# Optimization experiments

Measured on AMD Instinct MI355X. Metric: run time of the kernel, lower is better.

Reference implementation:

```python
import jax, jax.numpy as jnp
import numpy as np

H, N, BSZ, L = 512, 64, 8, 2048
DT_MIN, DT_MAX = 1e-3, 1e-1


def _hippo_dplr(n_state):
    """HiPPO-LegS -> DPLR (Lambda, P, B) init, as in the Annotated S4."""
    n = np.arange(n_state, dtype=np.float64)
    p = np.sqrt(n + 0.5)                      # low-rank factor P
    pm = np.sqrt(1.0 + 2.0 * n)
    A = np.tril(pm[:, None] * pm[None, :]) - np.diag(n)
    A = -A                                    # HiPPO-LegS A
    S = A + p[:, None] * p[None, :]           # normal part (skew-symmetric + cI)
    lam_real = np.mean(np.diagonal(S)) * np.ones(n_state)
    lam_imag, V = np.linalg.eigh(S * -1j)
    Lam = lam_real + 1j * lam_imag
    B = np.sqrt(2.0 * n + 1.0)
    return Lam, V.conj().T @ p, V.conj().T @ B


def setup_inputs() -> dict:
    key = jax.random.key(0)
    k1, k2, k3, k4, k5 = jax.random.split(key, 5)
    Lam, P, B = _hippo_dplr(N)
    return {
        "u": jax.random.normal(k1, (BSZ, L, H), dtype=jnp.float32),
        "Lambda_real": jnp.asarray(Lam.real, jnp.float32),
        "Lambda_imag": jnp.asarray(Lam.imag, jnp.float32),
        "P_real": jnp.asarray(P.real, jnp.float32),
        "P_imag": jnp.asarray(P.imag, jnp.float32),
        "B_real": jnp.asarray(B.real, jnp.float32),
        "B_imag": jnp.asarray(B.imag, jnp.float32),
        "C_real": jax.random.normal(k2, (H, N), jnp.float32) * 0.5,
        "C_imag": jax.random.normal(k3, (H, N), jnp.float32) * 0.5,
        "log_dt": jax.random.uniform(k4, (H,), jnp.float32,
                                     float(np.log(DT_MIN)), float(np.log(DT_MAX))),
        "D": jax.random.normal(k5, (H,), jnp.float32) * 0.01,
    }


def _s4_forward(u, Lr, Li, Pr, Pi, Br, Bi, Cr, Ci, log_dt, D):
    Lam = (Lr + 1j * Li).astype(jnp.complex64)   # (N,)
    P = (Pr + 1j * Pi).astype(jnp.complex64)     # (N,)
    B = (Br + 1j * Bi).astype(jnp.complex64)     # (N,)
    C = (Cr + 1j * Ci).astype(jnp.complex64)     # (H, N)
    l_len = u.shape[1]
    dt = jnp.exp(log_dt)                         # (H,)

    # --- DPLR kernel via Cauchy-kernel generating function (bilinear disc),
    # batched over all H channels instead of the per-channel Python loop. ---
    omega = jnp.exp(-2j * jnp.pi * jnp.arange(l_len, dtype=jnp.float32) / l_len)
    omega = omega.astype(jnp.complex64)          # roots of unity, (L,)
    g = (2.0 / dt)[:, None].astype(jnp.complex64) * ((1.0 - omega) / (1.0 + omega))[None, :]  # (H, L)
    c2 = 2.0 / (1.0 + omega)                     # (L,)
    r = 1.0 / (g[:, :, None] - Lam[None, None, :])  # Cauchy resolvent (H, L, N)
    Cc = jnp.conj(C)                             # (H, N)
    Qc = jnp.conj(P)                             # (N,)
    k00 = jnp.einsum('hn,hln->hl', Cc * B[None, :], r)
    k01 = jnp.einsum('hn,hln->hl', Cc * P[None, :], r)
    k10 = jnp.einsum('n,hln->hl', Qc * B, r)
    k11 = jnp.einsum('n,hln->hl', Qc * P, r)
    at_roots = c2[None, :] * (k00 - k01 * k10 / (1.0 + k11))  # (H, L)
    K = jnp.fft.ifft(at_roots, axis=-1).real.astype(u.dtype)  # (H, L) conv kernel

    # --- causal FFT convolution per channel ---
    x = jnp.swapaxes(u, -1, -2)                  # (B, H, L)
    n_fft = 2 * l_len
    Xf = jnp.fft.rfft(x, n=n_fft)
    Kf = jnp.fft.rfft(K, n=n_fft)
    y = jnp.fft.irfft(Xf * Kf[None], n=n_fft)[..., :l_len]
    y = y + x * D[None, :, None]                 # skip connection
    return jnp.swapaxes(y, -1, -2)               # (B, L, H)


def reference(u, Lambda_real, Lambda_imag, P_real, P_imag, B_real, B_imag,
              C_real, C_imag, log_dt, D):
    return _s4_forward(u, Lambda_real, Lambda_imag, P_real, P_imag,
                       B_real, B_imag, C_real, C_imag, log_dt, D)
```

## Files before the change

### kernel.cpp

```cpp
#include <hip/hip_runtime.h>
#include <math.h>

#define LSEQ 2048
#define HCH  512
#define NST  64
#define NBATCH 8
#define PIf 3.14159265358979f

#define PHYS(i) ((i) + ((i) >> 3))
#define LDSN 2304

__device__ __forceinline__ float2 cmul(float2 a, float2 b) {
    return make_float2(a.x * b.x - a.y * b.y, a.x * b.y + a.y * b.x);
}
__device__ __forceinline__ float2 cadd(float2 a, float2 b) { return make_float2(a.x + b.x, a.y + b.y); }
__device__ __forceinline__ float2 csub(float2 a, float2 b) { return make_float2(a.x - b.x, a.y - b.y); }
__device__ __forceinline__ float2 csq(float2 a) { return make_float2(a.x * a.x - a.y * a.y, 2.f * a.x * a.y); }
template<int INV>
__device__ __forceinline__ float2 rot90(float2 a) {
    return INV ? make_float2(-a.y, a.x) : make_float2(a.y, -a.x);
}

template<int INV, int STAGE>
__device__ __forceinline__ void radix8_pass(const float2* __restrict__ src,
                                            float2* __restrict__ dst, int tid)
{
    const int Ns  = 1 << STAGE;
    const int lam = tid & (Ns - 1);
    const int G   = ((tid >> STAGE) << (STAGE + 3)) + lam;

    float2 x0 = src[PHYS(tid)];
    float2 x1 = src[PHYS(tid + 256)];
    float2 x2 = src[PHYS(tid + 512)];
    float2 x3 = src[PHYS(tid + 768)];
    float2 x4 = src[PHYS(tid + 1024)];
    float2 x5 = src[PHYS(tid + 1280)];
    float2 x6 = src[PHYS(tid + 1536)];
    float2 x7 = src[PHYS(tid + 1792)];

    const float SGN = INV ? 1.f : -1.f;
    float sn, cs;
    __sincosf(SGN * (PIf / (float)(4 * Ns)) * (float)lam, &sn, &cs);
    const float2 T3 = make_float2(cs, sn);
    const float2 T2 = csq(T3);
    const float2 T1 = csq(T2);
    const float r2 = 0.70710678118f;
    const float2 U = cmul(T3, make_float2(r2, SGN * r2));

    float2 t;
    t = cmul(T1, x4); float2 a0 = cadd(x0, t), a4 = csub(x0, t);
    t = cmul(T1, x5); float2 a1 = cadd(x1, t), a5 = csub(x1, t);
    t = cmul(T1, x6); float2 a2 = cadd(x2, t), a6 = csub(x2, t);
    t = cmul(T1, x7); float2 a3 = cadd(x3, t), a7 = csub(x3, t);
    t = cmul(T2, a2);             float2 b0 = cadd(a0, t), b2 = csub(a0, t);
    t = cmul(T2, a3);             float2 b1 = cadd(a1, t), b3 = csub(a1, t);
    t = rot90<INV>(cmul(T2, a6)); float2 b4 = cadd(a4, t), b6 = csub(a4, t);
    t = rot90<INV>(cmul(T2, a7)); float2 b5 = cadd(a5, t), b7 = csub(a5, t);
    t = cmul(T3, b1);             dst[PHYS(G)]          = cadd(b0, t); dst[PHYS(G + 4 * Ns)] = csub(b0, t);
    t = rot90<INV>(cmul(T3, b3)); dst[PHYS(G + 2 * Ns)] = cadd(b2, t); dst[PHYS(G + 6 * Ns)] = csub(b2, t);
    t = cmul(U, b5);              dst[PHYS(G + Ns)]     = cadd(b4, t); dst[PHYS(G + 5 * Ns)] = csub(b4, t);
    t = rot90<INV>(cmul(U, b7));  dst[PHYS(G + 3 * Ns)] = cadd(b6, t); dst[PHYS(G + 7 * Ns)] = csub(b6, t);
}

template<int INV>
__device__ float2* fft2048(float2* bufA, float2* bufB)
{
    const int tid = threadIdx.x;
    __syncthreads();
    radix8_pass<INV, 0>(bufA, bufB, tid);
    __syncthreads();
    radix8_pass<INV, 3>(bufB, bufA, tid);
    __syncthreads();
    radix8_pass<INV, 6>(bufA, bufB, tid);
    __syncthreads();
    const float SGN = INV ? 1.f : -1.f;
#pragma unroll
    for (int q = 0; q < 2; ++q) {
        const int j = tid + (q << 8);
        float2 A  = bufB[PHYS(j)];
        float2 C  = bufB[PHYS(j + 512)];
        float2 B  = bufB[PHYS(j + 1024)];
        float2 Dd = bufB[PHYS(j + 1536)];
        float sn, cs;
        __sincosf(SGN * (PIf / 1024.f) * (float)j, &sn, &cs);
        const float2 v = make_float2(cs, sn);
        const float2 w = csq(v);
        float2 t = cmul(w, B);  float2 m1 = cadd(A, t), m2 = csub(A, t);
        t = cmul(w, Dd);        float2 m3 = cadd(C, t), m4 = csub(C, t);
        const float2 t3 = cmul(v, m3);
        const float2 t4 = rot90<INV>(cmul(v, m4));
        bufA[PHYS(j)]        = cadd(m1, t3);
        bufA[PHYS(j + 1024)] = csub(m1, t3);
        bufA[PHYS(j + 512)]  = cadd(m2, t4);
        bufA[PHYS(j + 1536)] = csub(m2, t4);
    }
    __syncthreads();
    return bufA;
}

__global__ __launch_bounds__(256, 4)
void s4_cauchy_kernel(const float* __restrict__ Lr, const float* __restrict__ Li,
                      const float* __restrict__ Pr, const float* __restrict__ Pi,
                      const float* __restrict__ Br, const float* __restrict__ Bi,
                      const float* __restrict__ Cr, const float* __restrict__ Ci,
                      const float* __restrict__ log_dt, float2* __restrict__ at_out)
{
    __shared__ float4 F0[NST];
    __shared__ float4 F1[NST];
    __shared__ float  q1s[NST];

    const int h    = blockIdx.x >> 1;
    const int half = blockIdx.x & 1;
    const int tid  = threadIdx.x;

    if (tid < NST) {
        const float pr = Pr[tid], pi = Pi[tid], br = Br[tid], bi = Bi[tid];
        const float cr = Cr[h * NST + tid], ci = Ci[h * NST + tid];
        F0[tid]  = make_float4(Lr[tid], Li[tid], cr * br + ci * bi, cr * bi - ci * br);
        F1[tid]  = make_float4(cr * pr + ci * pi, cr * pi - ci * pr,
                               pr * br + pi * bi, pr * bi - pi * br);
        q1s[tid] = pr * pr + pi * pi;
    }
    __syncthreads();

    const float dt = expf(log_dt[h]);
    const float a  = 2.0f / dt;

    float tt[4], g[4];
#pragma unroll
    for (int p = 0; p < 4; ++p) {
        const int l = (half << 10) + (p << 8) + tid;
        tt[p] = tanf(PIf * (float)l * (1.0f / 2048.0f));
        g[p]  = a * tt[p];
    }

    float k00r[4], k00i[4], k01r[4], k01i[4];
    float k10r[4], k10i[4], k11r[4], k11i[4];
#pragma unroll
    for (int p = 0; p < 4; ++p) {
        k00r[p] = 0.f; k00i[p] = 0.f; k01r[p] = 0.f; k01i[p] = 0.f;
        k10r[p] = 0.f; k10i[p] = 0.f; k11r[p] = 0.f; k11i[p] = 0.f;
    }

#pragma unroll 2
    for (int n = 0; n < NST; ++n) {
        const float4 f0 = F0[n];
        const float4 f1 = F1[n];
        const float q1 = q1s[n];
        const float x  = -f0.x;
        const float x2 = x * x;
#pragma unroll
        for (int p = 0; p < 4; ++p) {
            const float y   = g[p] - f0.y;
            const float inv = __builtin_amdgcn_rcpf(fmaf(y, y, x2));
            const float rr  = x * inv;
            const float ri  = -y * inv;
            k00r[p] = fmaf(f0.z, rr, fmaf(-f0.w, ri, k00r[p]));
            k00i[p] = fmaf(f0.z, ri, fmaf( f0.w, rr, k00i[p]));
            k01r[p] = fmaf(f1.x, rr, fmaf(-f1.y, ri, k01r[p]));
            k01i[p] = fmaf(f1.x, ri, fmaf( f1.y, rr, k01i[p]));
            k10r[p] = fmaf(f1.z, rr, fmaf(-f1.w, ri, k10r[p]));
            k10i[p] = fmaf(f1.z, ri, fmaf( f1.w, rr, k10i[p]));
            k11r[p] = fmaf(q1, rr, k11r[p]);
            k11i[p] = fmaf(q1, ri, k11i[p]);
        }
    }

    float2* __restrict__ row = at_out + (size_t)h * 2048;
#pragma unroll
    for (int p = 0; p < 4; ++p) {
        const int l = (half << 10) + (p << 8) + tid;
        const float dr = 1.0f + k11r[p], di = k11i[p];
        const float dinv = __builtin_amdgcn_rcpf(fmaf(dr, dr, di * di));
        const float pr_ = k01r[p] * k10r[p] - k01i[p] * k10i[p];
        const float pi_ = k01r[p] * k10i[p] + k01i[p] * k10r[p];
        const float qr = (pr_ * dr + pi_ * di) * dinv;
        const float qi = (pi_ * dr - pr_ * di) * dinv;
        const float sr = k00r[p] - qr, si = k00i[p] - qi;
        row[l] = make_float2(fmaf(-tt[p], si, sr), fmaf(tt[p], sr, si));
    }
}

__global__ __launch_bounds__(256, 4)
void s4_kf_kernel(const float2* __restrict__ at_in, float2* __restrict__ Kf)
{
    __shared__ float2 bufA[LDSN];
    __shared__ float2 bufB[LDSN];

    const int h   = blockIdx.x;
    const int tid = threadIdx.x;
    const float2* __restrict__ at = at_in + (size_t)h * 2048;

    for (int q = 0; q < 8; ++q) {
        const int l = tid + (q << 8);
        bufA[PHYS(l)] = at[l];
    }

    float2* Kt = fft2048<1>(bufA, bufB);

    const float sc = 1.0f / 2048.0f;
    for (int n = tid; n < 1024; n += 256)
        bufB[PHYS(n)] = make_float2(Kt[PHYS(2 * n)].x * sc, Kt[PHYS(2 * n + 1)].x * sc);
    for (int n = 1024 + tid; n < 2048; n += 256)
        bufB[PHYS(n)] = make_float2(0.f, 0.f);

    float2* Z = fft2048<0>(bufB, bufA);

    float2* __restrict__ out = Kf + (size_t)h * 2049;
    for (int k = tid; k < 1024; k += 256) {
        const float2 Zk = Z[PHYS(k)];
        const float2 Zm = Z[PHYS((2048 - k) & 2047)];
        const float zer = 0.5f * (Zk.x + Zm.x), zei = 0.5f * (Zk.y - Zm.y);
        const float zdr = Zk.x - Zm.x,         zdi = Zk.y + Zm.y;
        const float zor = 0.5f * zdi,          zoi = -0.5f * zdr;
        float s, c;
        __sincosf(-PIf * (float)k * (1.0f / 2048.0f), &s, &c);
        const float txr = c * zor - s * zoi;
        const float txi = c * zoi + s * zor;
        out[k] = make_float2(zer + txr, zei + txi);
        if (k > 0) {
            out[2048 - k] = make_float2(zer - txr, txi - zei);
        } else {
            out[2048] = make_float2(Zk.x - Zk.y, 0.f);
        }
    }
    if (tid == 0) {
        const float2 z = Z[PHYS(1024)];
        out[1024] = make_float2(z.x, -z.y);
    }
}

__global__ __launch_bounds__(256, 4)
void s4_conv_kernel(const float* __restrict__ u, float* ws_rows,
                    const float2* __restrict__ Kf, const float* __restrict__ Dv,
                    float* __restrict__ out, int fastpath)
{
    __shared__ float2 bufA[LDSN];
    __shared__ float2 bufB[LDSN];
    __shared__ float2 yfN;

    const int bh  = blockIdx.x;
    const int b   = bh >> 9;
    const int h   = bh & 511;
    const int tid = threadIdx.x;

    if (fastpath) {
        const float2* rowv = (const float2*)(ws_rows + (size_t)bh * LSEQ);
        for (int n = tid; n < 1024; n += 256) bufA[PHYS(n)] = rowv[n];
    } else {
        const float* ub = u + (size_t)b * LSEQ * HCH + h;
        for (int n = tid; n < 1024; n += 256)
            bufA[PHYS(n)] = make_float2(ub[(size_t)(2 * n) * HCH],
                                        ub[(size_t)(2 * n + 1) * HCH]);
    }
    for (int n = 1024 + tid; n < 2048; n += 256) bufA[PHYS(n)] = make_float2(0.f, 0.f);

    float2* Z  = fft2048<0>(bufA, bufB);
    float2* NB = bufB;
    const float2* __restrict__ kf = Kf + (size_t)h * 2049;

    for (int k = tid; k < 1024; k += 256) {
        const float2 Zk = Z[PHYS(k)];
        const float2 Zm = Z[PHYS((2048 - k) & 2047)];
        const float zer = 0.5f * (Zk.x + Zm.x), zei = 0.5f * (Zk.y - Zm.y);
        const float zdr = Zk.x - Zm.x,          zdi = Zk.y + Zm.y;
        const float zor = 0.5f * zdi,           zoi = -0.5f * zdr;
        float s, c;
        __sincosf(-PIf * (float)k * (1.0f / 2048.0f), &s, &c);
        const float txr = c * zor - s * zoi;
        const float txi = c * zoi + s * zor;
        const float xr = zer + txr, xi = zei + txi;
        const float2 kk = kf[k];
        NB[PHYS(k)] = make_float2(xr * kk.x - xi * kk.y, xr * kk.y + xi * kk.x);
        if (k > 0) {
            const float mr = zer - txr, mi = txi - zei;
            const float2 km = kf[2048 - k];
            NB[PHYS(2048 - k)] = make_float2(mr * km.x - mi * km.y,
                                             mr * km.y + mi * km.x);
        } else {
            const float x2048 = Zk.x - Zk.y;
            const float2 k2 = kf[2048];
            yfN = make_float2(x2048 * k2.x, x2048 * k2.y);
        }
    }
    if (tid == 0) {
        const float2 z  = Z[PHYS(1024)];
        const float2 kk = kf[1024];
        NB[PHYS(1024)] = make_float2(z.x * kk.x + z.y * kk.y,
                                     z.x * kk.y - z.y * kk.x);
    }
    __syncthreads();

    for (int k = tid; k < 1024; k += 256) {
        const float2 Yk = NB[PHYS(k)];
        const float2 Ym = (k == 0) ? yfN : NB[PHYS(2048 - k)];
        const float yer = 0.5f * (Yk.x + Ym.x), yei = 0.5f * (Yk.y - Ym.y);
        const float ydr = Yk.x - Ym.x,          ydi = Yk.y + Ym.y;
        float s, c;
        __sincosf(PIf * (float)k * (1.0f / 2048.0f), &s, &c);
        const float yor = 0.5f * (c * ydr - s * ydi);
        const float yoi = 0.5f * (c * ydi + s * ydr);
        bufA[PHYS(k)] = make_float2(yer - yoi, yei + yor);
        if (k > 0) {
            const float yer2 = 0.5f * (Ym.x + Yk.x), yei2 = 0.5f * (Ym.y - Yk.y);
            const float ydr2 = Ym.x - Yk.x,          ydi2 = Ym.y + Yk.y;
            const float yor2 = 0.5f * (-c * ydr2 - s * ydi2);
            const float yoi2 = 0.5f * (-c * ydi2 + s * ydr2);
            bufA[PHYS(2048 - k)] = make_float2(yer2 - yoi2, yei2 + yor2);
        }
    }
    if (tid == 0) {
        const float2 Y = NB[PHYS(1024)];
        bufA[PHYS(1024)] = make_float2(Y.x, -Y.y);
    }

    float2* w = fft2048<1>(bufA, bufB);
    const float Dh = Dv[h];
    const float sc = 1.0f / 2048.0f;
    if (fastpath) {
        float2* rowv = (float2*)(ws_rows + (size_t)bh * LSEQ);
        for (int n = tid; n < 1024; n += 256) {
            const float2 wv = w[PHYS(n)];
            const float2 xv = rowv[n];
            rowv[n] = make_float2(wv.x * sc + Dh * xv.x,
                                  wv.y * sc + Dh * xv.y);
        }
    } else {
        const float* ub = u + (size_t)b * LSEQ * HCH + h;
        float* ob = out + (size_t)b * LSEQ * HCH + h;
        for (int n = tid; n < 1024; n += 256) {
            const float2 wv = w[PHYS(n)];
            ob[(size_t)(2 * n) * HCH]     = wv.x * sc + Dh * ub[(size_t)(2 * n) * HCH];
            ob[(size_t)(2 * n + 1) * HCH] = wv.y * sc + Dh * ub[(size_t)(2 * n + 1) * HCH];
        }
    }
}

__global__ __launch_bounds__(256)
void transpose_kernel(const float* __restrict__ in, float* __restrict__ out,
                      int rows, int cols)
{
    __shared__ float tile[32][33];
    const int b  = blockIdx.z;
    const int r0 = blockIdx.y << 5;
    const int c0 = blockIdx.x << 5;
    const size_t base = (size_t)b * rows * cols;
    const int tx = threadIdx.x & 31;
    const int ty = threadIdx.x >> 5;
#pragma unroll
    for (int i = 0; i < 32; i += 8)
        tile[ty + i][tx] = in[base + (size_t)(r0 + ty + i) * cols + (c0 + tx)];
    __syncthreads();
#pragma unroll
    for (int i = 0; i < 32; i += 8)
        out[base + (size_t)(c0 + ty + i) * rows + (r0 + tx)] = tile[tx][ty + i];
}

extern "C" void kernel_launch(void* const* d_in, const int* in_sizes, int n_in,
                              void* d_out, int out_size, void* d_ws, size_t ws_size,
                              hipStream_t stream)
{
    (void)in_sizes; (void)n_in; (void)out_size;
    const float* u  = (const float*)d_in[0];
    const float* Lr = (const float*)d_in[1];
    const float* Li = (const float*)d_in[2];
    const float* Pr = (const float*)d_in[3];
    const float* Pi = (const float*)d_in[4];
    const float* Br = (const float*)d_in[5];
    const float* Bi = (const float*)d_in[6];
    const float* Cr = (const float*)d_in[7];
    const float* Ci = (const float*)d_in[8];
    const float* ld = (const float*)d_in[9];
    const float* Dv = (const float*)d_in[10];
    float* out = (float*)d_out;

    const size_t UT_BYTES = (size_t)NBATCH * HCH * LSEQ * sizeof(float);
    const size_t KF_BYTES = (size_t)HCH * 2049 * sizeof(float2);
    const int fast = (ws_size >= UT_BYTES + KF_BYTES) ? 1 : 0;

    float*  ut;
    float2* Kf;
    if (fast) { ut = (float*)d_ws; Kf = (float2*)((char*)d_ws + UT_BYTES); }
    else      { ut = (float*)d_ws; Kf = (float2*)d_ws; }

    float2* at = (float2*)d_out;

    hipLaunchKernelGGL(s4_cauchy_kernel, dim3(HCH * 2), dim3(256), 0, stream,
                       Lr, Li, Pr, Pi, Br, Bi, Cr, Ci, ld, at);
    hipLaunchKernelGGL(s4_kf_kernel, dim3(HCH), dim3(256), 0, stream, at, Kf);
    if (fast) {
        hipLaunchKernelGGL(transpose_kernel, dim3(HCH / 32, LSEQ / 32, NBATCH),
                           dim3(256), 0, stream, u, ut, LSEQ, HCH);
    }
    hipLaunchKernelGGL(s4_conv_kernel, dim3(NBATCH * HCH), dim3(256), 0, stream,
                       u, fast ? ut : nullptr, Kf, Dv, out, fast);
    if (fast) {
        hipLaunchKernelGGL(transpose_kernel, dim3(LSEQ / 32, HCH / 32, NBATCH),
                           dim3(256), 0, stream, ut, out, HCH, LSEQ);
    }
}
```

Measured before the change: 115.9 us.

## Make conv-kernel FFTs in-place with a single LDS buffer for higher occupancy

```diff
diff --git a/kernel.cpp b/kernel.cpp
--- a/kernel.cpp
+++ b/kernel.cpp
@@ -98,6 +98,82 @@
     return bufA;
 }
 
+template<int INV, int STAGE>
+__device__ __forceinline__ void radix8_inplace(float2* __restrict__ buf, int tid)
+{
+    __syncthreads();
+    float2 x0 = buf[PHYS(tid)];
+    float2 x1 = buf[PHYS(tid + 256)];
+    float2 x2 = buf[PHYS(tid + 512)];
+    float2 x3 = buf[PHYS(tid + 768)];
+    float2 x4 = buf[PHYS(tid + 1024)];
+    float2 x5 = buf[PHYS(tid + 1280)];
+    float2 x6 = buf[PHYS(tid + 1536)];
+    float2 x7 = buf[PHYS(tid + 1792)];
+    __syncthreads();
+
+    const int Ns  = 1 << STAGE;
+    const int lam = tid & (Ns - 1);
+    const int G   = ((tid >> STAGE) << (STAGE + 3)) + lam;
+    const float SGN = INV ? 1.f : -1.f;
+    float sn, cs;
+    __sincosf(SGN * (PIf / (float)(4 * Ns)) * (float)lam, &sn, &cs);
+    const float2 T3 = make_float2(cs, sn);
+    const float2 T2 = csq(T3);
+    const float2 T1 = csq(T2);
+    const float r2 = 0.70710678118f;
+    const float2 U = cmul(T3, make_float2(r2, SGN * r2));
+    float2 t;
+    t = cmul(T1, x4); float2 a0 = cadd(x0, t), a4 = csub(x0, t);
+    t = cmul(T1, x5); float2 a1 = cadd(x1, t), a5 = csub(x1, t);
+    t = cmul(T1, x6); float2 a2 = cadd(x2, t), a6 = csub(x2, t);
+    t = cmul(T1, x7); float2 a3 = cadd(x3, t), a7 = csub(x3, t);
+    t = cmul(T2, a2);             float2 b0 = cadd(a0, t), b2 = csub(a0, t);
+    t = cmul(T2, a3);             float2 b1 = cadd(a1, t), b3 = csub(a1, t);
+    t = rot90<INV>(cmul(T2, a6)); float2 b4 = cadd(a4, t), b6 = csub(a4, t);
+    t = rot90<INV>(cmul(T2, a7)); float2 b5 = cadd(a5, t), b7 = csub(a5, t);
+    t = cmul(T3, b1);             buf[PHYS(G)]          = cadd(b0, t); buf[PHYS(G + 4 * Ns)] = csub(b0, t);
+    t = rot90<INV>(cmul(T3, b3)); buf[PHYS(G + 2 * Ns)] = cadd(b2, t); buf[PHYS(G + 6 * Ns)] = csub(b2, t);
+    t = cmul(U, b5);              buf[PHYS(G + Ns)]     = cadd(b4, t); buf[PHYS(G + 5 * Ns)] = csub(b4, t);
+    t = rot90<INV>(cmul(U, b7));  buf[PHYS(G + 3 * Ns)] = cadd(b6, t); buf[PHYS(G + 7 * Ns)] = csub(b6, t);
+}
+
+template<int INV>
+__device__ __forceinline__ void radix4_inplace(float2* __restrict__ buf, int tid)
+{
+    __syncthreads();
+    const float SGN = INV ? 1.f : -1.f;
+#pragma unroll
+    for (int q = 0; q < 2; ++q) {
+        const int j = tid + (q << 8);
+        float2 A  = buf[PHYS(j)];
+        float2 C  = buf[PHYS(j + 512)];
+        float2 B  = buf[PHYS(j + 1024)];
+        float2 Dd = buf[PHYS(j + 1536)];
+        float sn, cs;
+        __sincosf(SGN * (PIf / 1024.f) * (float)j, &sn, &cs);
+        const float2 v = make_float2(cs, sn);
+        const float2 w = csq(v);
+        float2 t = cmul(w, B);  float2 m1 = cadd(A, t), m2 = csub(A, t);
+        t = cmul(w, Dd);        float2 m3 = cadd(C, t), m4 = csub(C, t);
+        const float2 t3 = cmul(v, m3);
+        const float2 t4 = rot90<INV>(cmul(v, m4));
+        buf[PHYS(j)]        = cadd(m1, t3);
+        buf[PHYS(j + 1024)] = csub(m1, t3);
+        buf[PHYS(j + 512)]  = cadd(m2, t4);
+        buf[PHYS(j + 1536)] = csub(m2, t4);
+    }
+}
+
+template<int INV>
+__device__ __forceinline__ void fft2048_ip(float2* buf, int tid)
+{
+    radix8_inplace<INV, 0>(buf, tid);
+    radix8_inplace<INV, 3>(buf, tid);
+    radix8_inplace<INV, 6>(buf, tid);
+    radix4_inplace<INV>(buf, tid);
+}
+
 __global__ __launch_bounds__(256, 4)
 void s4_cauchy_kernel(const float* __restrict__ Lr, const float* __restrict__ Li,
                       const float* __restrict__ Pr, const float* __restrict__ Pi,
@@ -230,13 +306,12 @@
     }
 }
 
-__global__ __launch_bounds__(256, 4)
+__global__ __launch_bounds__(256, 6)
 void s4_conv_kernel(const float* __restrict__ u, float* ws_rows,
                     const float2* __restrict__ Kf, const float* __restrict__ Dv,
                     float* __restrict__ out, int fastpath)
 {
-    __shared__ float2 bufA[LDSN];
-    __shared__ float2 bufB[LDSN];
+    __shared__ float2 buf[LDSN];
     __shared__ float2 yfN;
 
     const int bh  = blockIdx.x;
@@ -246,24 +321,35 @@
 
     if (fastpath) {
         const float2* rowv = (const float2*)(ws_rows + (size_t)bh * LSEQ);
-        for (int n = tid; n < 1024; n += 256) bufA[PHYS(n)] = rowv[n];
+        for (int n = tid; n < 1024; n += 256) buf[PHYS(n)] = rowv[n];
     } else {
         const float* ub = u + (size_t)b * LSEQ * HCH + h;
         for (int n = tid; n < 1024; n += 256)
-            bufA[PHYS(n)] = make_float2(ub[(size_t)(2 * n) * HCH],
-                                        ub[(size_t)(2 * n + 1) * HCH]);
-    }
-    for (int n = 1024 + tid; n < 2048; n += 256) bufA[PHYS(n)] = make_float2(0.f, 0.f);
-
-    float2* Z  = fft2048<0>(bufA, bufB);
-    float2* NB = bufB;
+            buf[PHYS(n)] = make_float2(ub[(size_t)(2 * n) * HCH],
+                                       ub[(size_t)(2 * n + 1) * HCH]);
+    }
+    for (int n = 1024 + tid; n < 2048; n += 256) buf[PHYS(n)] = make_float2(0.f, 0.f);
+
+    fft2048_ip<0>(buf, tid);
+
     const float2* __restrict__ kf = Kf + (size_t)h * 2049;
 
-    for (int k = tid; k < 1024; k += 256) {
-        const float2 Zk = Z[PHYS(k)];
-        const float2 Zm = Z[PHYS((2048 - k) & 2047)];
-        const float zer = 0.5f * (Zk.x + Zm.x), zei = 0.5f * (Zk.y - Zm.y);
-        const float zdr = Zk.x - Zm.x,          zdi = Zk.y + Zm.y;
+    __syncthreads();
+    float2 Zk[4], Zm[4], Z1024v;
+#pragma unroll
+    for (int q = 0; q < 4; ++q) {
+        const int k = tid + (q << 8);
+        Zk[q] = buf[PHYS(k)];
+        Zm[q] = buf[PHYS((2048 - k) & 2047)];
+    }
+    if (tid == 0) Z1024v = buf[PHYS(1024)];
+    __syncthreads();
+#pragma unroll
+    for (int q = 0; q < 4; ++q) {
+        const int k = tid + (q << 8);
+        const float2 zk = Zk[q], zm = Zm[q];
+        const float zer = 0.5f * (zk.x + zm.x), zei = 0.5f * (zk.y - zm.y);
+        const float zdr = zk.x - zm.x,          zdi = zk.y + zm.y;
         const float zor = 0.5f * zdi,           zoi = -0.5f * zdr;
         float s, c;
         __sincosf(-PIf * (float)k * (1.0f / 2048.0f), &s, &c);
@@ -271,56 +357,66 @@
         const float txi = c * zoi + s * zor;
         const float xr = zer + txr, xi = zei + txi;
         const float2 kk = kf[k];
-        NB[PHYS(k)] = make_float2(xr * kk.x - xi * kk.y, xr * kk.y + xi * kk.x);
+        buf[PHYS(k)] = make_float2(xr * kk.x - xi * kk.y, xr * kk.y + xi * kk.x);
         if (k > 0) {
             const float mr = zer - txr, mi = txi - zei;
             const float2 km = kf[2048 - k];
-            NB[PHYS(2048 - k)] = make_float2(mr * km.x - mi * km.y,
-                                             mr * km.y + mi * km.x);
+            buf[PHYS(2048 - k)] = make_float2(mr * km.x - mi * km.y,
+                                              mr * km.y + mi * km.x);
         } else {
-            const float x2048 = Zk.x - Zk.y;
+            const float x2048 = zk.x - zk.y;
             const float2 k2 = kf[2048];
             yfN = make_float2(x2048 * k2.x, x2048 * k2.y);
         }
     }
     if (tid == 0) {
-        const float2 z  = Z[PHYS(1024)];
         const float2 kk = kf[1024];
-        NB[PHYS(1024)] = make_float2(z.x * kk.x + z.y * kk.y,
-                                     z.x * kk.y - z.y * kk.x);
-    }
-    __syncthreads();
-
-    for (int k = tid; k < 1024; k += 256) {
-        const float2 Yk = NB[PHYS(k)];
-        const float2 Ym = (k == 0) ? yfN : NB[PHYS(2048 - k)];
-        const float yer = 0.5f * (Yk.x + Ym.x), yei = 0.5f * (Yk.y - Ym.y);
-        const float ydr = Yk.x - Ym.x,          ydi = Yk.y + Ym.y;
+        buf[PHYS(1024)] = make_float2(Z1024v.x * kk.x + Z1024v.y * kk.y,
+                                      Z1024v.x * kk.y - Z1024v.y * kk.x);
+    }
+
+    __syncthreads();
+    float2 Yk[4], Ym[4], Y1024v;
+#pragma unroll
+    for (int q = 0; q < 4; ++q) {
+        const int k = tid + (q << 8);
+        Yk[q] = buf[PHYS(k)];
+        Ym[q] = (k == 0) ? yfN : buf[PHYS(2048 - k)];
+    }
+    if (tid == 0) Y1024v = buf[PHYS(1024)];
+    __syncthreads();
+#pragma unroll
+    for (int q = 0; q < 4; ++q) {
+        const int k = tid + (q << 8);
+        const float2 yk = Yk[q], ym = Ym[q];
+        const float yer = 0.5f * (yk.x + ym.x), yei = 0.5f * (yk.y - ym.y);
+        const float ydr = yk.x - ym.x,          ydi = yk.y + ym.y;
         float s, c;
         __sincosf(PIf * (float)k * (1.0f / 2048.0f), &s, &c);
         const float yor = 0.5f * (c * ydr - s * ydi);
         const float yoi = 0.5f * (c * ydi + s * ydr);
-        bufA[PHYS(k)] = make_float2(yer - yoi, yei + yor);
+        buf[PHYS(k)] = make_float2(yer - yoi, yei + yor);
         if (k > 0) {
-            const float yer2 = 0.5f * (Ym.x + Yk.x), yei2 = 0.5f * (Ym.y - Yk.y);
-            const float ydr2 = Ym.x - Yk.x,          ydi2 = Ym.y + Yk.y;
+            const float yer2 = 0.5f * (ym.x + yk.x), yei2 = 0.5f * (ym.y - yk.y);
+            const float ydr2 = ym.x - yk.x,          ydi2 = ym.y + yk.y;
             const float yor2 = 0.5f * (-c * ydr2 - s * ydi2);
             const float yoi2 = 0.5f * (-c * ydi2 + s * ydr2);
-            bufA[PHYS(2048 - k)] = make_float2(yer2 - yoi2, yei2 + yor2);
+            buf[PHYS(2048 - k)] = make_float2(yer2 - yoi2, yei2 + yor2);
         }
     }
     if (tid == 0) {
-        const float2 Y = NB[PHYS(1024)];
-        bufA[PHYS(1024)] = make_float2(Y.x, -Y.y);
-    }
-
-    float2* w = fft2048<1>(bufA, bufB);
+        buf[PHYS(1024)] = make_float2(Y1024v.x, -Y1024v.y);
+    }
+
+    fft2048_ip<1>(buf, tid);
+
+    __syncthreads();
     const float Dh = Dv[h];
     const float sc = 1.0f / 2048.0f;
     if (fastpath) {
         float2* rowv = (float2*)(ws_rows + (size_t)bh * LSEQ);
         for (int n = tid; n < 1024; n += 256) {
-            const float2 wv = w[PHYS(n)];
+            const float2 wv = buf[PHYS(n)];
             const float2 xv = rowv[n];
             rowv[n] = make_float2(wv.x * sc + Dh * xv.x,
                                   wv.y * sc + Dh * xv.y);
@@ -329,7 +425,7 @@
         const float* ub = u + (size_t)b * LSEQ * HCH + h;
         float* ob = out + (size_t)b * LSEQ * HCH + h;
         for (int n = tid; n < 1024; n += 256) {
-            const float2 wv = w[PHYS(n)];
+            const float2 wv = buf[PHYS(n)];
             ob[(size_t)(2 * n) * HCH]     = wv.x * sc + Dh * ub[(size_t)(2 * n) * HCH];
             ob[(size_t)(2 * n + 1) * HCH] = wv.y * sc + Dh * ub[(size_t)(2 * n + 1) * HCH];
         }
```

Result: faster. 110.6 us (-4.5%).

## Pack two batches into one complex 4096-point FFT and drop transposes

Applied to the files above, without the earlier changes.

```diff
diff --git a/kernel.cpp b/kernel.cpp
--- a/kernel.cpp
+++ b/kernel.cpp
@@ -9,6 +9,7 @@
 
 #define PHYS(i) ((i) + ((i) >> 3))
 #define LDSN 2304
+#define LDSN4 4608
 
 __device__ __forceinline__ float2 cmul(float2 a, float2 b) {
     return make_float2(a.x * b.x - a.y * b.y, a.x * b.y + a.y * b.x);
@@ -98,6 +99,46 @@
     return bufA;
 }
 
+template<int INV, int STAGE>
+__device__ __forceinline__ void radix8_ip4096(float2* __restrict__ buf, int tid)
+{
+    __syncthreads();
+    float2 x0 = buf[PHYS(tid)];
+    float2 x1 = buf[PHYS(tid + 512)];
+    float2 x2 = buf[PHYS(tid + 1024)];
+    float2 x3 = buf[PHYS(tid + 1536)];
+    float2 x4 = buf[PHYS(tid + 2048)];
+    float2 x5 = buf[PHYS(tid + 2560)];
+    float2 x6 = buf[PHYS(tid + 3072)];
+    float2 x7 = buf[PHYS(tid + 3584)];
+    __syncthreads();
+
+    const int Ns  = 1 << STAGE;
+    const int lam = tid & (Ns - 1);
+    const int G   = ((tid >> STAGE) << (STAGE + 3)) + lam;
+    const float SGN = INV ? 1.f : -1.f;
+    float sn, cs;
+    __sincosf(SGN * (PIf / (float)(4 * Ns)) * (float)lam, &sn, &cs);
+    const float2 T3 = make_float2(cs, sn);
+    const float2 T2 = csq(T3);
+    const float2 T1 = csq(T2);
+    const float r2 = 0.70710678118f;
+    const float2 U = cmul(T3, make_float2(r2, SGN * r2));
+    float2 t;
+    t = cmul(T1, x4); float2 a0 = cadd(x0, t), a4 = csub(x0, t);
+    t = cmul(T1, x5); float2 a1 = cadd(x1, t), a5 = csub(x1, t);
+    t = cmul(T1, x6); float2 a2 = cadd(x2, t), a6 = csub(x2, t);
+    t = cmul(T1, x7); float2 a3 = cadd(x3, t), a7 = csub(x3, t);
+    t = cmul(T2, a2);             float2 b0 = cadd(a0, t), b2 = csub(a0, t);
+    t = cmul(T2, a3);             float2 b1 = cadd(a1, t), b3 = csub(a1, t);
+    t = rot90<INV>(cmul(T2, a6)); float2 b4 = cadd(a4, t), b6 = csub(a4, t);
+    t = rot90<INV>(cmul(T2, a7)); float2 b5 = cadd(a5, t), b7 = csub(a5, t);
+    t = cmul(T3, b1);             buf[PHYS(G)]          = cadd(b0, t); buf[PHYS(G + 4 * Ns)] = csub(b0, t);
+    t = rot90<INV>(cmul(T3, b3)); buf[PHYS(G + 2 * Ns)] = cadd(b2, t); buf[PHYS(G + 6 * Ns)] = csub(b2, t);
+    t = cmul(U, b5);              buf[PHYS(G + Ns)]     = cadd(b4, t); buf[PHYS(G + 5 * Ns)] = csub(b4, t);
+    t = rot90<INV>(cmul(U, b7));  buf[PHYS(G + 3 * Ns)] = cadd(b6, t); buf[PHYS(G + 7 * Ns)] = csub(b6, t);
+}
+
 __global__ __launch_bounds__(256, 4)
 void s4_cauchy_kernel(const float* __restrict__ Lr, const float* __restrict__ Li,
                       const float* __restrict__ Pr, const float* __restrict__ Pi,
@@ -230,137 +271,71 @@
     }
 }
 
-__global__ __launch_bounds__(256, 4)
-void s4_conv_kernel(const float* __restrict__ u, float* ws_rows,
-                    const float2* __restrict__ Kf, const float* __restrict__ Dv,
-                    float* __restrict__ out, int fastpath)
-{
-    __shared__ float2 bufA[LDSN];
-    __shared__ float2 bufB[LDSN];
-    __shared__ float2 yfN;
-
-    const int bh  = blockIdx.x;
-    const int b   = bh >> 9;
-    const int h   = bh & 511;
+__global__ __launch_bounds__(512, 8)
+void s4_conv_kernel(const float* __restrict__ u, const float2* __restrict__ Kf,
+                    const float* __restrict__ Dv, float* __restrict__ out)
+{
+    __shared__ float2 buf[LDSN4];
+
+    const int bp  = blockIdx.x;
+    const int h   = bp & (HCH - 1);
+    const int b0  = (bp >> 9) << 1;
     const int tid = threadIdx.x;
 
-    if (fastpath) {
-        const float2* rowv = (const float2*)(ws_rows + (size_t)bh * LSEQ);
-        for (int n = tid; n < 1024; n += 256) bufA[PHYS(n)] = rowv[n];
-    } else {
-        const float* ub = u + (size_t)b * LSEQ * HCH + h;
-        for (int n = tid; n < 1024; n += 256)
-            bufA[PHYS(n)] = make_float2(ub[(size_t)(2 * n) * HCH],
-                                        ub[(size_t)(2 * n + 1) * HCH]);
-    }
-    for (int n = 1024 + tid; n < 2048; n += 256) bufA[PHYS(n)] = make_float2(0.f, 0.f);
-
-    float2* Z  = fft2048<0>(bufA, bufB);
-    float2* NB = bufB;
+    const float* __restrict__ u0 = u + (size_t)b0 * LSEQ * HCH + h;
+    const float* __restrict__ u1 = u0 + (size_t)LSEQ * HCH;
+
+#pragma unroll
+    for (int m = 0; m < 4; ++m) {
+        const int n = tid + (m << 9);
+        buf[PHYS(n)]        = make_float2(u0[(size_t)n * HCH], u1[(size_t)n * HCH]);
+        buf[PHYS(n + 2048)] = make_float2(0.f, 0.f);
+    }
+
+    radix8_ip4096<0, 0>(buf, tid);
+    radix8_ip4096<0, 3>(buf, tid);
+    radix8_ip4096<0, 6>(buf, tid);
+    radix8_ip4096<0, 9>(buf, tid);
+
     const float2* __restrict__ kf = Kf + (size_t)h * 2049;
-
-    for (int k = tid; k < 1024; k += 256) {
-        const float2 Zk = Z[PHYS(k)];
-        const float2 Zm = Z[PHYS((2048 - k) & 2047)];
-        const float zer = 0.5f * (Zk.x + Zm.x), zei = 0.5f * (Zk.y - Zm.y);
-        const float zdr = Zk.x - Zm.x,          zdi = Zk.y + Zm.y;
-        const float zor = 0.5f * zdi,           zoi = -0.5f * zdr;
-        float s, c;
-        __sincosf(-PIf * (float)k * (1.0f / 2048.0f), &s, &c);
-        const float txr = c * zor - s * zoi;
-        const float txi = c * zoi + s * zor;
-        const float xr = zer + txr, xi = zei + txi;
-        const float2 kk = kf[k];
-        NB[PHYS(k)] = make_float2(xr * kk.x - xi * kk.y, xr * kk.y + xi * kk.x);
-        if (k > 0) {
-            const float mr = zer - txr, mi = txi - zei;
-            const float2 km = kf[2048 - k];
-            NB[PHYS(2048 - k)] = make_float2(mr * km.x - mi * km.y,
-                                             mr * km.y + mi * km.x);
+    __syncthreads();
+#pragma unroll
+    for (int m = 0; m < 8; ++m) {
+        const int k = tid + (m << 9);
+        float2 C;
+        if (k <= 2048) {
+            C = kf[k];
         } else {
-            const float x2048 = Zk.x - Zk.y;
-            const float2 k2 = kf[2048];
-            yfN = make_float2(x2048 * k2.x, x2048 * k2.y);
+            const float2 km = kf[4096 - k];
+            C = make_float2(km.x, -km.y);
         }
-    }
-    if (tid == 0) {
-        const float2 z  = Z[PHYS(1024)];
-        const float2 kk = kf[1024];
-        NB[PHYS(1024)] = make_float2(z.x * kk.x + z.y * kk.y,
-                                     z.x * kk.y - z.y * kk.x);
-    }
-    __syncthreads();
-
-    for (int k = tid; k < 1024; k += 256) {
-        const float2 Yk = NB[PHYS(k)];
-        const float2 Ym = (k == 0) ? yfN : NB[PHYS(2048 - k)];
-        const float yer = 0.5f * (Yk.x + Ym.x), yei = 0.5f * (Yk.y - Ym.y);
-        const float ydr = Yk.x - Ym.x,          ydi = Yk.y + Ym.y;
-        float s, c;
-        __sincosf(PIf * (float)k * (1.0f / 2048.0f), &s, &c);
-        const float yor = 0.5f * (c * ydr - s * ydi);
-        const float yoi = 0.5f * (c * ydi + s * ydr);
-        bufA[PHYS(k)] = make_float2(yer - yoi, yei + yor);
-        if (k > 0) {
-            const float yer2 = 0.5f * (Ym.x + Yk.x), yei2 = 0.5f * (Ym.y - Yk.y);
-            const float ydr2 = Ym.x - Yk.x,          ydi2 = Ym.y + Yk.y;
-            const float yor2 = 0.5f * (-c * ydr2 - s * ydi2);
-            const float yoi2 = 0.5f * (-c * ydi2 + s * ydr2);
-            bufA[PHYS(2048 - k)] = make_float2(yer2 - yoi2, yei2 + yor2);
-        }
-    }
-    if (tid == 0) {
-        const float2 Y = NB[PHYS(1024)];
-        bufA[PHYS(1024)] = make_float2(Y.x, -Y.y);
-    }
-
-    float2* w = fft2048<1>(bufA, bufB);
+        buf[PHYS(k)] = cmul(buf[PHYS(k)], C);
+    }
+
+    radix8_ip4096<1, 0>(buf, tid);
+    radix8_ip4096<1, 3>(buf, tid);
+    radix8_ip4096<1, 6>(buf, tid);
+    radix8_ip4096<1, 9>(buf, tid);
+
+    __syncthreads();
     const float Dh = Dv[h];
-    const float sc = 1.0f / 2048.0f;
-    if (fastpath) {
-        float2* rowv = (float2*)(ws_rows + (size_t)bh * LSEQ);
-        for (int n = tid; n < 1024; n += 256) {
-            const float2 wv = w[PHYS(n)];
-            const float2 xv = rowv[n];
-            rowv[n] = make_float2(wv.x * sc + Dh * xv.x,
-                                  wv.y * sc + Dh * xv.y);
-        }
-    } else {
-        const float* ub = u + (size_t)b * LSEQ * HCH + h;
-        float* ob = out + (size_t)b * LSEQ * HCH + h;
-        for (int n = tid; n < 1024; n += 256) {
-            const float2 wv = w[PHYS(n)];
-            ob[(size_t)(2 * n) * HCH]     = wv.x * sc + Dh * ub[(size_t)(2 * n) * HCH];
-            ob[(size_t)(2 * n + 1) * HCH] = wv.y * sc + Dh * ub[(size_t)(2 * n + 1) * HCH];
-        }
-    }
-}
-
-__global__ __launch_bounds__(256)
-void transpose_kernel(const float* __restrict__ in, float* __restrict__ out,
-                      int rows, int cols)
-{
-    __shared__ float tile[32][33];
-    const int b  = blockIdx.z;
-    const int r0 = blockIdx.y << 5;
-    const int c0 = blockIdx.x << 5;
-    const size_t base = (size_t)b * rows * cols;
-    const int tx = threadIdx.x & 31;
-    const int ty = threadIdx.x >> 5;
-#pragma unroll
-    for (int i = 0; i < 32; i += 8)
-        tile[ty + i][tx] = in[base + (size_t)(r0 + ty + i) * cols + (c0 + tx)];
-    __syncthreads();
-#pragma unroll
-    for (int i = 0; i < 32; i += 8)
-        out[base + (size_t)(c0 + ty + i) * rows + (r0 + tx)] = tile[tx][ty + i];
+    const float sc = 1.0f / 4096.0f;
+    float* __restrict__ o0 = out + (size_t)b0 * LSEQ * HCH + h;
+    float* __restrict__ o1 = o0 + (size_t)LSEQ * HCH;
+#pragma unroll
+    for (int m = 0; m < 4; ++m) {
+        const int n = tid + (m << 9);
+        const float2 w = buf[PHYS(n)];
+        o0[(size_t)n * HCH] = fmaf(Dh, u0[(size_t)n * HCH], w.x * sc);
+        o1[(size_t)n * HCH] = fmaf(Dh, u1[(size_t)n * HCH], w.y * sc);
+    }
 }
 
 extern "C" void kernel_launch(void* const* d_in, const int* in_sizes, int n_in,
                               void* d_out, int out_size, void* d_ws, size_t ws_size,
                               hipStream_t stream)
 {
-    (void)in_sizes; (void)n_in; (void)out_size;
+    (void)in_sizes; (void)n_in; (void)out_size; (void)ws_size;
     const float* u  = (const float*)d_in[0];
     const float* Lr = (const float*)d_in[1];
     const float* Li = (const float*)d_in[2];
@@ -374,28 +349,12 @@
     const float* Dv = (const float*)d_in[10];
     float* out = (float*)d_out;
 
-    const size_t UT_BYTES = (size_t)NBATCH * HCH * LSEQ * sizeof(float);
-    const size_t KF_BYTES = (size_t)HCH * 2049 * sizeof(float2);
-    const int fast = (ws_size >= UT_BYTES + KF_BYTES) ? 1 : 0;
-
-    float*  ut;
-    float2* Kf;
-    if (fast) { ut = (float*)d_ws; Kf = (float2*)((char*)d_ws + UT_BYTES); }
-    else      { ut = (float*)d_ws; Kf = (float2*)d_ws; }
-
+    float2* Kf = (float2*)d_ws;
     float2* at = (float2*)d_out;
 
     hipLaunchKernelGGL(s4_cauchy_kernel, dim3(HCH * 2), dim3(256), 0, stream,
                        Lr, Li, Pr, Pi, Br, Bi, Cr, Ci, ld, at);
     hipLaunchKernelGGL(s4_kf_kernel, dim3(HCH), dim3(256), 0, stream, at, Kf);
-    if (fast) {
-        hipLaunchKernelGGL(transpose_kernel, dim3(HCH / 32, LSEQ / 32, NBATCH),
-                           dim3(256), 0, stream, u, ut, LSEQ, HCH);
-    }
-    hipLaunchKernelGGL(s4_conv_kernel, dim3(NBATCH * HCH), dim3(256), 0, stream,
-                       u, fast ? ut : nullptr, Kf, Dv, out, fast);
-    if (fast) {
-        hipLaunchKernelGGL(transpose_kernel, dim3(LSEQ / 32, HCH / 32, NBATCH),
-                           dim3(256), 0, stream, ut, out, HCH, LSEQ);
-    }
-}
+    hipLaunchKernelGGL(s4_conv_kernel, dim3(NBATCH / 2 * HCH), dim3(512), 0, stream,
+                       u, Kf, Dv, out);
+}
```

Result: slower. 326.2 us (+181.5%).
